# Kernel optimization log

Hardware: AMD Instinct MI355X
Metric: run time of the kernel (lower is better)

Reference implementation:

```python
import jax, jax.numpy as jnp
import numpy as np

HID = 256   # hiddenDims
QD = 64     # queryDims
B = 16      # number of segments
LQ = 2048   # query tokens per segment
LH = 2048   # key/value tokens per segment
EPS = 1e-5


def _layer_norm(x, w, b):
    m = jnp.mean(x, axis=-1, keepdims=True)
    v = jnp.mean((x - m) ** 2, axis=-1, keepdims=True)
    return (x - m) / jnp.sqrt(v + EPS) * w + b


def setup_inputs() -> dict:
    key = jax.random.key(0)
    ks = jax.random.split(key, 8)
    q = jax.random.normal(ks[0], (B * LQ, HID), jnp.float32)
    h = jax.random.normal(ks[1], (B * LH, HID), jnp.float32)
    s = 1.0 / np.sqrt(HID)
    WQ = jax.random.normal(ks[2], (QD, HID), jnp.float32) * s
    WK = jax.random.normal(ks[3], (QD, HID), jnp.float32) * s
    WV = jax.random.normal(ks[4], (HID, HID), jnp.float32) * s
    fc_w = jax.random.normal(ks[5], (HID, HID), jnp.float32) * s
    fc_b = jax.random.normal(ks[6], (HID,), jnp.float32) * 0.01
    norm0_w = jnp.ones((HID,), jnp.float32)
    norm0_b = jnp.zeros((HID,), jnp.float32)
    norm1_w = jnp.ones((HID,), jnp.float32)
    norm1_b = jnp.zeros((HID,), jnp.float32)
    qlens = jnp.full((B,), LQ, jnp.int32)
    hlens = jnp.full((B,), LH, jnp.int32)
    return {"q": q, "h": h, "WQ": WQ, "WK": WK, "WV": WV,
            "fc_w": fc_w, "fc_b": fc_b,
            "norm0_w": norm0_w, "norm0_b": norm0_b,
            "norm1_w": norm1_w, "norm1_b": norm1_b,
            "qlens": qlens, "hlens": hlens}


def reference(q, h, WQ, WK, WV, fc_w, fc_b,
              norm0_w, norm0_b, norm1_w, norm1_b, qlens, hlens):
    # segments are equal-length, so the ragged per-segment loop is exactly
    # batched block-diagonal attention over [B, L, D] views.
    nb = qlens.shape[0]
    Lq = q.shape[0] // nb
    Lh = h.shape[0] // hlens.shape[0]
    D = q.shape[-1]
    qq = (q @ WQ.T).reshape(nb, Lq, -1)          # [B, Lq, QD]
    k = (h @ WK.T).reshape(nb, Lh, -1)           # [B, Lh, QD]
    v = (h @ WV.T).reshape(nb, Lh, D)            # [B, Lh, D]
    scale = 1.0 / jnp.sqrt(jnp.asarray(qq.shape[-1], jnp.float32))
    a = jax.nn.softmax(jnp.einsum('bqc,bkc->bqk', qq, k) * scale, axis=-1)
    att = jnp.einsum('bqk,bkd->bqd', a, v).reshape(-1, D)  # concat of segments
    x = _layer_norm(q + att, norm0_w, norm0_b)
    hres = x @ fc_w.T + fc_b
    return _layer_norm(x + jax.nn.relu(hres), norm1_w, norm1_b)
```

## Files before the change

### kernel.cpp

```cpp
#include <hip/hip_runtime.h>
#include <hip/hip_bf16.h>

#define HID 256
#define QD 64
#define NSEG 16
#define SLQ 2048
#define SLH 2048


typedef __attribute__((ext_vector_type(8))) short bf16x8;
typedef __attribute__((ext_vector_type(8))) __bf16 bf16x8b;
typedef __attribute__((ext_vector_type(4))) float f32x4;
typedef __attribute__((ext_vector_type(4))) short s16x4;

#define BAR_LDS() asm volatile("s_waitcnt lgkmcnt(0)\n\ts_barrier" ::: "memory")

static __device__ __forceinline__ f32x4 mfma16(bf16x8 a, bf16x8 b, f32x4 c) {
  return __builtin_amdgcn_mfma_f32_16x16x32_bf16(
      __builtin_bit_cast(bf16x8b, a), __builtin_bit_cast(bf16x8b, b), c, 0, 0, 0);
}

static __device__ __forceinline__ short f2bf(float x) {
  union { float f; unsigned u; } v; v.f = x;
  unsigned r = v.u + 0x7fffu + ((v.u >> 16) & 1u);
  return (short)(r >> 16);
}

static __device__ __forceinline__ float bf2f(short s) {
  union { unsigned u; float f; } v;
  v.u = ((unsigned)(unsigned short)s) << 16;
  return v.f;
}

static __device__ __forceinline__ void pack_w(const float* __restrict__ s,
                                              short* __restrict__ d, int i) {
  int j = i & 7, l16 = (i >> 3) & 15, quad = (i >> 7) & 3, ks = (i >> 9) & 7,
      n = i >> 12;
  d[i] = f2bf(s[(size_t)(n * 16 + l16) * HID + ks * 32 + quad * 8 + j]);
}

__global__ __launch_bounds__(256) void cast4_kernel(const float* __restrict__ s0, short* __restrict__ d0, int n0,
                                                    const float* __restrict__ s1, short* __restrict__ d1, int n1,
                                                    const float* __restrict__ s2, short* __restrict__ d2, int n2,
                                                    const float* __restrict__ s3, short* __restrict__ d3, int n3) {
  int i = blockIdx.x * 256 + threadIdx.x;
  if (i < n0) pack_w(s0, d0, i);
  int j = i - n0;
  if (j >= 0 && j < n1) pack_w(s1, d1, j);
  int k = j - n1;
  if (k >= 0 && k < n2) pack_w(s2, d2, k);
  int l = k - n2;
  if (l >= 0 && l < n3) pack_w(s3, d3, l);
}

__global__ __launch_bounds__(256, 4) void proj_kernel(const float* __restrict__ q,
                                                      const float* __restrict__ h,
                                                      const short* __restrict__ wqb,
                                                      const short* __restrict__ wkb,
                                                      const short* __restrict__ wvb,
                                                      short* __restrict__ qq,
                                                      short* __restrict__ kb,
                                                      short* __restrict__ vt) {
  __shared__ short hb[64][264];
  int wave = threadIdx.x >> 6, lane = threadIdx.x & 63;
  int quad = lane >> 4, l16 = lane & 15;
  int mw = wave * 16;

  if (blockIdx.x < 512) {
    int m0 = blockIdx.x * 64;
#pragma unroll
    for (int i = 0; i < 16; ++i) {
      int idx = i * 256 + threadIdx.x;
      int row = idx >> 6, col = (idx & 63) * 4;
      f32x4 v = *(const f32x4*)(h + (size_t)(m0 + row) * HID + col);
      s16x4 pk;
#pragma unroll
      for (int j = 0; j < 4; ++j) pk[j] = f2bf(v[j]);
      *(s16x4*)&hb[row][col] = pk;
    }
    __syncthreads();
    f32x4 kacc[4];
    f32x4 vacc[16];
#pragma unroll
    for (int n = 0; n < 4; ++n) kacc[n] = f32x4{0.f, 0.f, 0.f, 0.f};
#pragma unroll
    for (int n = 0; n < 16; ++n) vacc[n] = f32x4{0.f, 0.f, 0.f, 0.f};
#pragma unroll
    for (int ks = 0; ks < 8; ++ks) {
      bf16x8 a = *(const bf16x8*)&hb[mw + l16][ks * 32 + quad * 8];
#pragma unroll
      for (int n = 0; n < 4; ++n) {
        bf16x8 b = *(const bf16x8*)(wkb + (size_t)((n * 8 + ks) * 64 + lane) * 8);
        kacc[n] = mfma16(a, b, kacc[n]);
      }
#pragma unroll
      for (int mt = 0; mt < 16; ++mt) {
        bf16x8 wf = *(const bf16x8*)(wvb + (size_t)((mt * 8 + ks) * 64 + lane) * 8);
        vacc[mt] = mfma16(wf, a, vacc[mt]);
      }
    }
    {
      char* kx = (char*)&hb[mw][0];
#pragma unroll
      for (int n = 0; n < 4; ++n)
#pragma unroll
        for (int r = 0; r < 4; ++r) {
          int k16 = quad * 4 + r;
          int bo = (k16 * 128 + (n * 16 + l16) * 2) ^ ((k16 & 7) << 4);
          *(short*)(kx + bo) = f2bf(kacc[n][r]);
        }
      asm volatile("s_waitcnt lgkmcnt(0)" ::: "memory");
      int seg = (m0 + mw) >> 11;
      int g = ((m0 + mw) & 2047) >> 4;
      short* kdst = kb + (size_t)seg * 131072 + (size_t)g * 1024 + lane * 8;
#pragma unroll
      for (int p = 0; p < 2; ++p) {
        int bo = (l16 * 128 + p * 64 + quad * 16) ^ ((l16 & 7) << 4);
        *(bf16x8*)(kdst + p * 512) = *(bf16x8*)(kx + bo);
      }
    }
    __syncthreads();
    {
      char* vbuf = (char*)&hb[0][0];
#pragma unroll
      for (int mt = 0; mt < 16; ++mt)
#pragma unroll
        for (int r = 0; r < 4; ++r) {
          int dv = mt * 16 + quad * 4 + r;
          int bo = (dv * 128 + (mw + l16) * 2) ^ ((dv & 7) << 4);
          *(short*)(vbuf + bo) = f2bf(vacc[mt][r]);
        }
      __syncthreads();
      int seg = m0 >> 11;
      int t0 = m0 & 2047;
      int kt = t0 >> 7;
      int ksb = (t0 >> 5) & 3;
      short* vdst = vt + (size_t)seg * 524288;
#pragma unroll
      for (int i = 0; i < 8; ++i) {
        int u = wave * 8 + i;
        int ksl = u >> 4, d16 = u & 15;
        int dim = d16 * 16 + l16;
        int bo = (dim * 128 + ksl * 64 + quad * 16) ^ ((dim & 7) << 4);
        size_t unit = (size_t)((kt * 4 + ksb + ksl) * 16 + d16);
        *(bf16x8*)(vdst + unit * 512 + lane * 8) = *(bf16x8*)(vbuf + bo);
      }
    }
  } else {
    int m0 = (blockIdx.x - 512) * 64;
#pragma unroll
    for (int i = 0; i < 16; ++i) {
      int idx = i * 256 + threadIdx.x;
      int row = idx >> 6, col = (idx & 63) * 4;
      f32x4 v = *(const f32x4*)(q + (size_t)(m0 + row) * HID + col);
      s16x4 pk;
#pragma unroll
      for (int j = 0; j < 4; ++j) pk[j] = f2bf(v[j]);
      *(s16x4*)&hb[row][col] = pk;
    }
    __syncthreads();
    f32x4 acc[4];
#pragma unroll
    for (int n = 0; n < 4; ++n) acc[n] = f32x4{0.f, 0.f, 0.f, 0.f};
#pragma unroll
    for (int ks = 0; ks < 8; ++ks) {
      bf16x8 a = *(const bf16x8*)&hb[mw + l16][ks * 32 + quad * 8];
#pragma unroll
      for (int n = 0; n < 4; ++n) {
        bf16x8 b = *(const bf16x8*)(wqb + (size_t)((n * 8 + ks) * 64 + lane) * 8);
        acc[n] = mfma16(a, b, acc[n]);
      }
    }
    {
      char* kx = (char*)&hb[mw][0];
#pragma unroll
      for (int n = 0; n < 4; ++n)
#pragma unroll
        for (int r = 0; r < 4; ++r) {
          int k16 = quad * 4 + r;
          int bo = (k16 * 128 + (n * 16 + l16) * 2) ^ ((k16 & 7) << 4);
          *(short*)(kx + bo) = f2bf(acc[n][r]);
        }
      asm volatile("s_waitcnt lgkmcnt(0)" ::: "memory");
      int g = (m0 >> 4) + wave;
      short* qdst = qq + (size_t)g * 1024 + lane * 8;
#pragma unroll
      for (int p = 0; p < 2; ++p) {
        int bo = (l16 * 128 + p * 64 + quad * 16) ^ ((l16 & 7) << 4);
        *(bf16x8*)(qdst + p * 512) = *(bf16x8*)(kx + bo);
      }
    }
  }
}

__global__ __launch_bounds__(512, 4) void attn_kernel(const short* __restrict__ qq,
                                                      const short* __restrict__ kb,
                                                      const short* __restrict__ vt,
                                                      const float* __restrict__ qres,
                                                      const float* __restrict__ n0w,
                                                      const float* __restrict__ n0b,
                                                      short* __restrict__ xb) {
  __shared__ short p_lds[2][64][136];
  __shared__ float plsum[4][2][16];
  int wave = threadIdx.x >> 6, lane = threadIdx.x & 63;
  int quad = lane >> 4, l16 = lane & 15;
  int qg = wave >> 1, kh = wave & 1;
  int b = blockIdx.x;
  int xcd = b & 7, li = b >> 3;
  int seg = xcd * 2 + (li >> 5);
  int tile = li & 31;
  int qrow0 = seg * SLQ + tile * 64;
  const short* kseg = kb + (size_t)seg * 131072;
  const short* vseg = vt + (size_t)seg * 524288;

  const short* qbase = qq + (size_t)((qrow0 >> 4) + qg) * 1024 + lane * 8;
  bf16x8 qf0 = *(const bf16x8*)qbase;
  bf16x8 qf1 = *(const bf16x8*)(qbase + 512);

  f32x4 o[4][2];
#pragma unroll
  for (int m = 0; m < 4; ++m)
#pragma unroll
    for (int n = 0; n < 2; ++n) o[m][n] = f32x4{0.f, 0.f, 0.f, 0.f};
  float lsum = 0.f;
  const float cexp = 0.125f * 1.44269504f;
  bf16x8 kpre[4][2];

#define LOADK(KT)                                                               \
  {                                                                             \
    _Pragma("unroll") for (int t = 0; t < 4; ++t) {                             \
      const short* kp = kseg + (size_t)((KT) * 8 + kh * 4 + t) * 1024 + lane * 8;\
      kpre[t][0] = *(const bf16x8*)kp;                                          \
      kpre[t][1] = *(const bf16x8*)(kp + 512);                                  \
    }                                                                           \
  }

#define S_PHASE(BUF)                                                            \
  {                                                                             \
    f32x4 s[4];                                                                 \
    _Pragma("unroll") for (int t = 0; t < 4; ++t) {                             \
      f32x4 a = f32x4{0.f, 0.f, 0.f, 0.f};                                      \
      a = mfma16(kpre[t][0], qf0, a);                                           \
      a = mfma16(kpre[t][1], qf1, a);                                           \
      s[t] = a;                                                                 \
    }                                                                           \
    _Pragma("unroll") for (int t = 0; t < 4; ++t) {                             \
      float p0 = __builtin_amdgcn_exp2f(s[t][0] * cexp);                        \
      float p1 = __builtin_amdgcn_exp2f(s[t][1] * cexp);                        \
      float p2 = __builtin_amdgcn_exp2f(s[t][2] * cexp);                        \
      float p3 = __builtin_amdgcn_exp2f(s[t][3] * cexp);                        \
      lsum += (p0 + p1) + (p2 + p3);                                            \
      s16x4 pk;                                                                 \
      pk[0] = f2bf(p0); pk[1] = f2bf(p1); pk[2] = f2bf(p2); pk[3] = f2bf(p3);   \
      *(s16x4*)&p_lds[BUF][qg * 16 + l16][kh * 64 + t * 16 + quad * 4] = pk;    \
    }                                                                           \
  }

#define PV_PHASE(KT, BUF)                                                       \
  {                                                                             \
    _Pragma("unroll") for (int ks = 0; ks < 4; ++ks) {                          \
      bf16x8 pf[4];                                                             \
      _Pragma("unroll") for (int m = 0; m < 4; ++m)                             \
        pf[m] = *(const bf16x8*)&p_lds[BUF][m * 16 + l16][ks * 32 + quad * 8];  \
      _Pragma("unroll") for (int n = 0; n < 2; ++n) {                           \
        const short* vp = vseg +                                                \
            ((size_t)((KT) * 4 + ks) * 16 + wave * 2 + n) * 512 + lane * 8;     \
        bf16x8 vf = *(const bf16x8*)vp;                                         \
        _Pragma("unroll") for (int m = 0; m < 4; ++m)                           \
          o[m][n] = mfma16(pf[m], vf, o[m][n]);                                 \
      }                                                                         \
    }                                                                           \
  }

  LOADK(tile & 15)
  S_PHASE(0)
  LOADK((tile + 1) & 15)
  BAR_LDS();
#pragma unroll 1
  for (int j = 1; j < 16; ++j) {
    S_PHASE(j & 1)
    if (j < 15) LOADK((tile + j + 1) & 15)
    PV_PHASE((tile + j - 1) & 15, (j - 1) & 1)
    BAR_LDS();
  }
  PV_PHASE((tile + 15) & 15, 1)

  lsum += __shfl_xor(lsum, 16);
  lsum += __shfl_xor(lsum, 32);

  BAR_LDS();
  if (lane < 16) plsum[qg][kh][lane] = lsum;
  short (*ob)[264] = (short(*)[264]) & p_lds[0][0][0];
#pragma unroll
  for (int m = 0; m < 4; ++m)
#pragma unroll
    for (int n = 0; n < 2; ++n)
#pragma unroll
      for (int r = 0; r < 4; ++r)
        ob[m * 16 + quad * 4 + r][wave * 32 + n * 16 + l16] = f2bf(o[m][n][r]);
  BAR_LDS();

  {
    int row = wave * 8 + (lane >> 3);
    int c0 = (lane & 7) * 32;
    float linv = 1.f / (plsum[row >> 4][0][row & 15] + plsum[row >> 4][1][row & 15]);
    float y[32];
    float s1 = 0.f, s2 = 0.f;
    const float* qp = qres + (size_t)(qrow0 + row) * HID + c0;
#pragma unroll
    for (int k = 0; k < 4; ++k) {
      bf16x8 ov = *(const bf16x8*)&ob[row][c0 + k * 8];
      f32x4 qa = *(const f32x4*)(qp + k * 8);
      f32x4 qb = *(const f32x4*)(qp + k * 8 + 4);
#pragma unroll
      for (int j = 0; j < 4; ++j) {
        float yv = qa[j] + bf2f(ov[j]) * linv;
        y[k * 8 + j] = yv;
        s1 += yv; s2 += yv * yv;
      }
#pragma unroll
      for (int j = 0; j < 4; ++j) {
        float yv = qb[j] + bf2f(ov[4 + j]) * linv;
        y[k * 8 + 4 + j] = yv;
        s1 += yv; s2 += yv * yv;
      }
    }
    s1 += __shfl_xor(s1, 1); s2 += __shfl_xor(s2, 1);
    s1 += __shfl_xor(s1, 2); s2 += __shfl_xor(s2, 2);
    s1 += __shfl_xor(s1, 4); s2 += __shfl_xor(s2, 4);
    float mean = s1 * (1.f / HID);
    float var = s2 * (1.f / HID) - mean * mean;
    float rstd = rsqrtf(var + 1e-5f);
    short* xp = xb + (size_t)(qrow0 + row) * HID + c0;
#pragma unroll
    for (int k = 0; k < 4; ++k) {
      f32x4 wa = *(const f32x4*)(n0w + c0 + k * 8);
      f32x4 wb = *(const f32x4*)(n0w + c0 + k * 8 + 4);
      f32x4 ba = *(const f32x4*)(n0b + c0 + k * 8);
      f32x4 bb = *(const f32x4*)(n0b + c0 + k * 8 + 4);
      s16x4 o0, o1;
#pragma unroll
      for (int j = 0; j < 4; ++j) {
        o0[j] = f2bf((y[k * 8 + j] - mean) * rstd * wa[j] + ba[j]);
        o1[j] = f2bf((y[k * 8 + 4 + j] - mean) * rstd * wb[j] + bb[j]);
      }
      *(s16x4*)(xp + k * 8) = o0;
      *(s16x4*)(xp + k * 8 + 4) = o1;
    }
  }
#undef LOADK
#undef S_PHASE
#undef PV_PHASE
}

__global__ __launch_bounds__(256) void fc_ln_kernel(const short* __restrict__ xb,
                                                    const short* __restrict__ fwb,
                                                    const float* __restrict__ fcb,
                                                    const float* __restrict__ w1,
                                                    const float* __restrict__ b1,
                                                    float* __restrict__ out) {
  __shared__ short xt[64][264];
  int m0 = blockIdx.x * 64;
#pragma unroll
  for (int i = 0; i < 8; ++i) {
    int idx = i * 256 + threadIdx.x;
    int row = idx >> 5, col = (idx & 31) * 8;
    bf16x8 v = *(const bf16x8*)(xb + (size_t)(m0 + row) * HID + col);
    *(bf16x8*)&xt[row][col] = v;
  }
  __syncthreads();
  int wave = threadIdx.x >> 6, lane = threadIdx.x & 63;
  int quad = lane >> 4, l16 = lane & 15;
  int mw = wave * 16;
  f32x4 acc[16];
#pragma unroll
  for (int n = 0; n < 16; ++n) acc[n] = f32x4{0.f, 0.f, 0.f, 0.f};
#pragma unroll
  for (int ks = 0; ks < 8; ++ks) {
    bf16x8 a = *(const bf16x8*)&xt[mw + l16][ks * 32 + quad * 8];
#pragma unroll
    for (int n = 0; n < 16; ++n) {
      bf16x8 b = *(const bf16x8*)(fwb + (size_t)((n * 8 + ks) * 64 + lane) * 8);
      acc[n] = mfma16(a, b, acc[n]);
    }
  }
#pragma unroll
  for (int r = 0; r < 4; ++r) {
    int lrow = mw + quad * 4 + r;
    int row = m0 + lrow;
    float yv[16];
    float s = 0.f, s2 = 0.f;
#pragma unroll
    for (int n = 0; n < 16; ++n) {
      int col = n * 16 + l16;
      float hres = acc[n][r] + fcb[col];
      hres = fmaxf(hres, 0.f);
      float y = bf2f(xt[lrow][col]) + hres;
      yv[n] = y;
      s += y;
      s2 += y * y;
    }
#pragma unroll
    for (int off = 1; off < 16; off <<= 1) {
      s += __shfl_xor(s, off);
      s2 += __shfl_xor(s2, off);
    }
    float mean = s * (1.f / HID);
    float var = s2 * (1.f / HID) - mean * mean;
    float rstd = rsqrtf(var + 1e-5f);
#pragma unroll
    for (int n = 0; n < 16; ++n) {
      int col = n * 16 + l16;
      out[(size_t)row * HID + col] = (yv[n] - mean) * rstd * w1[col] + b1[col];
    }
  }
}

extern "C" void kernel_launch(void* const* d_in, const int* in_sizes, int n_in,
                              void* d_out, int out_size, void* d_ws, size_t ws_size,
                              hipStream_t stream) {
  const float* q = (const float*)d_in[0];
  const float* h = (const float*)d_in[1];
  const float* WQ = (const float*)d_in[2];
  const float* WK = (const float*)d_in[3];
  const float* WV = (const float*)d_in[4];
  const float* fc_w = (const float*)d_in[5];
  const float* fc_b = (const float*)d_in[6];
  const float* n0w = (const float*)d_in[7];
  const float* n0b = (const float*)d_in[8];
  const float* n1w = (const float*)d_in[9];
  const float* n1b = (const float*)d_in[10];

  char* ws = (char*)d_ws;
  short* qq = (short*)(ws);
  short* kb = (short*)(ws + ((size_t)4 << 20));
  short* vt = (short*)(ws + ((size_t)8 << 20));
  short* xb = (short*)(ws + ((size_t)24 << 20));
  short* wqb = (short*)(ws + ((size_t)40 << 20));
  short* wkb = (short*)(ws + ((size_t)40 << 20) + 32 * 1024);
  short* wvb = (short*)(ws + ((size_t)40 << 20) + 64 * 1024);
  short* fwb = (short*)(ws + ((size_t)40 << 20) + 192 * 1024);

  cast4_kernel<<<640, 256, 0, stream>>>(WQ, wqb, QD * HID, WK, wkb, QD * HID,
                                        WV, wvb, HID * HID, fc_w, fwb, HID * HID);
  proj_kernel<<<1024, 256, 0, stream>>>(q, h, wqb, wkb, wvb, qq, kb, vt);
  attn_kernel<<<512, 512, 0, stream>>>(qq, kb, vt, q, n0w, n0b, xb);
  fc_ln_kernel<<<512, 256, 0, stream>>>(xb, fwb, fc_b, n1w, n1b, (float*)d_out);
}
```

Measured before the change: 271.9 us.

## Fuse Q projection and FC+LayerNorm epilogue into attention kernel

Moves the query projection out of the projection kernel into the attention kernel's prologue, where each block projects its own 64 query rows through LDS. The fc GEMM, ReLU, residual and second LayerNorm are folded into the attention epilogue, with row statistics reduced across wave halves through shared memory, and the separate fc_ln kernel is removed. This drops one launch plus the round trips of the qq and xb intermediates through global memory. In exchange the attention kernel uses more LDS and registers, which may lower occupancy and lengthen its serial prologue and epilogue.

```diff
diff --git a/kernel.cpp b/kernel.cpp
--- a/kernel.cpp
+++ b/kernel.cpp
@@ -53,155 +53,111 @@
   if (l >= 0 && l < n3) pack_w(s3, d3, l);
 }
 
-__global__ __launch_bounds__(256, 4) void proj_kernel(const float* __restrict__ q,
-                                                      const float* __restrict__ h,
-                                                      const short* __restrict__ wqb,
-                                                      const short* __restrict__ wkb,
-                                                      const short* __restrict__ wvb,
-                                                      short* __restrict__ qq,
-                                                      short* __restrict__ kb,
-                                                      short* __restrict__ vt) {
+__global__ __launch_bounds__(256, 4) void proj_kv_kernel(const float* __restrict__ h,
+                                                         const short* __restrict__ wkb,
+                                                         const short* __restrict__ wvb,
+                                                         short* __restrict__ kb,
+                                                         short* __restrict__ vt) {
   __shared__ short hb[64][264];
   int wave = threadIdx.x >> 6, lane = threadIdx.x & 63;
   int quad = lane >> 4, l16 = lane & 15;
   int mw = wave * 16;
-
-  if (blockIdx.x < 512) {
-    int m0 = blockIdx.x * 64;
-#pragma unroll
-    for (int i = 0; i < 16; ++i) {
-      int idx = i * 256 + threadIdx.x;
-      int row = idx >> 6, col = (idx & 63) * 4;
-      f32x4 v = *(const f32x4*)(h + (size_t)(m0 + row) * HID + col);
-      s16x4 pk;
-#pragma unroll
-      for (int j = 0; j < 4; ++j) pk[j] = f2bf(v[j]);
-      *(s16x4*)&hb[row][col] = pk;
-    }
+  int m0 = blockIdx.x * 64;
+#pragma unroll
+  for (int i = 0; i < 16; ++i) {
+    int idx = i * 256 + threadIdx.x;
+    int row = idx >> 6, col = (idx & 63) * 4;
+    f32x4 v = *(const f32x4*)(h + (size_t)(m0 + row) * HID + col);
+    s16x4 pk;
+#pragma unroll
+    for (int j = 0; j < 4; ++j) pk[j] = f2bf(v[j]);
+    *(s16x4*)&hb[row][col] = pk;
+  }
+  __syncthreads();
+  f32x4 kacc[4];
+  f32x4 vacc[16];
+#pragma unroll
+  for (int n = 0; n < 4; ++n) kacc[n] = f32x4{0.f, 0.f, 0.f, 0.f};
+#pragma unroll
+  for (int n = 0; n < 16; ++n) vacc[n] = f32x4{0.f, 0.f, 0.f, 0.f};
+#pragma unroll
+  for (int ks = 0; ks < 8; ++ks) {
+    bf16x8 a = *(const bf16x8*)&hb[mw + l16][ks * 32 + quad * 8];
+#pragma unroll
+    for (int n = 0; n < 4; ++n) {
+      bf16x8 b = *(const bf16x8*)(wkb + (size_t)((n * 8 + ks) * 64 + lane) * 8);
+      kacc[n] = mfma16(a, b, kacc[n]);
+    }
+#pragma unroll
+    for (int mt = 0; mt < 16; ++mt) {
+      bf16x8 wf = *(const bf16x8*)(wvb + (size_t)((mt * 8 + ks) * 64 + lane) * 8);
+      vacc[mt] = mfma16(wf, a, vacc[mt]);
+    }
+  }
+  {
+    char* kx = (char*)&hb[mw][0];
+#pragma unroll
+    for (int n = 0; n < 4; ++n)
+#pragma unroll
+      for (int r = 0; r < 4; ++r) {
+        int k16 = quad * 4 + r;
+        int bo = (k16 * 128 + (n * 16 + l16) * 2) ^ ((k16 & 7) << 4);
+        *(short*)(kx + bo) = f2bf(kacc[n][r]);
+      }
+    asm volatile("s_waitcnt lgkmcnt(0)" ::: "memory");
+    int seg = (m0 + mw) >> 11;
+    int g = ((m0 + mw) & 2047) >> 4;
+    short* kdst = kb + (size_t)seg * 131072 + (size_t)g * 1024 + lane * 8;
+#pragma unroll
+    for (int p = 0; p < 2; ++p) {
+      int bo = (l16 * 128 + p * 64 + quad * 16) ^ ((l16 & 7) << 4);
+      *(bf16x8*)(kdst + p * 512) = *(bf16x8*)(kx + bo);
+    }
+  }
+  __syncthreads();
+  {
+    char* vbuf = (char*)&hb[0][0];
+#pragma unroll
+    for (int mt = 0; mt < 16; ++mt)
+#pragma unroll
+      for (int r = 0; r < 4; ++r) {
+        int dv = mt * 16 + quad * 4 + r;
+        int bo = (dv * 128 + (mw + l16) * 2) ^ ((dv & 7) << 4);
+        *(short*)(vbuf + bo) = f2bf(vacc[mt][r]);
+      }
     __syncthreads();
-    f32x4 kacc[4];
-    f32x4 vacc[16];
-#pragma unroll
-    for (int n = 0; n < 4; ++n) kacc[n] = f32x4{0.f, 0.f, 0.f, 0.f};
-#pragma unroll
-    for (int n = 0; n < 16; ++n) vacc[n] = f32x4{0.f, 0.f, 0.f, 0.f};
-#pragma unroll
-    for (int ks = 0; ks < 8; ++ks) {
-      bf16x8 a = *(const bf16x8*)&hb[mw + l16][ks * 32 + quad * 8];
-#pragma unroll
-      for (int n = 0; n < 4; ++n) {
-        bf16x8 b = *(const bf16x8*)(wkb + (size_t)((n * 8 + ks) * 64 + lane) * 8);
-        kacc[n] = mfma16(a, b, kacc[n]);
-      }
-#pragma unroll
-      for (int mt = 0; mt < 16; ++mt) {
-        bf16x8 wf = *(const bf16x8*)(wvb + (size_t)((mt * 8 + ks) * 64 + lane) * 8);
-        vacc[mt] = mfma16(wf, a, vacc[mt]);
-      }
-    }
-    {
-      char* kx = (char*)&hb[mw][0];
-#pragma unroll
-      for (int n = 0; n < 4; ++n)
-#pragma unroll
-        for (int r = 0; r < 4; ++r) {
-          int k16 = quad * 4 + r;
-          int bo = (k16 * 128 + (n * 16 + l16) * 2) ^ ((k16 & 7) << 4);
-          *(short*)(kx + bo) = f2bf(kacc[n][r]);
-        }
-      asm volatile("s_waitcnt lgkmcnt(0)" ::: "memory");
-      int seg = (m0 + mw) >> 11;
-      int g = ((m0 + mw) & 2047) >> 4;
-      short* kdst = kb + (size_t)seg * 131072 + (size_t)g * 1024 + lane * 8;
-#pragma unroll
-      for (int p = 0; p < 2; ++p) {
-        int bo = (l16 * 128 + p * 64 + quad * 16) ^ ((l16 & 7) << 4);
-        *(bf16x8*)(kdst + p * 512) = *(bf16x8*)(kx + bo);
-      }
-    }
-    __syncthreads();
-    {
-      char* vbuf = (char*)&hb[0][0];
-#pragma unroll
-      for (int mt = 0; mt < 16; ++mt)
-#pragma unroll
-        for (int r = 0; r < 4; ++r) {
-          int dv = mt * 16 + quad * 4 + r;
-          int bo = (dv * 128 + (mw + l16) * 2) ^ ((dv & 7) << 4);
-          *(short*)(vbuf + bo) = f2bf(vacc[mt][r]);
-        }
-      __syncthreads();
-      int seg = m0 >> 11;
-      int t0 = m0 & 2047;
-      int kt = t0 >> 7;
-      int ksb = (t0 >> 5) & 3;
-      short* vdst = vt + (size_t)seg * 524288;
-#pragma unroll
-      for (int i = 0; i < 8; ++i) {
-        int u = wave * 8 + i;
-        int ksl = u >> 4, d16 = u & 15;
-        int dim = d16 * 16 + l16;
-        int bo = (dim * 128 + ksl * 64 + quad * 16) ^ ((dim & 7) << 4);
-        size_t unit = (size_t)((kt * 4 + ksb + ksl) * 16 + d16);
-        *(bf16x8*)(vdst + unit * 512 + lane * 8) = *(bf16x8*)(vbuf + bo);
-      }
-    }
-  } else {
-    int m0 = (blockIdx.x - 512) * 64;
-#pragma unroll
-    for (int i = 0; i < 16; ++i) {
-      int idx = i * 256 + threadIdx.x;
-      int row = idx >> 6, col = (idx & 63) * 4;
-      f32x4 v = *(const f32x4*)(q + (size_t)(m0 + row) * HID + col);
-      s16x4 pk;
-#pragma unroll
-      for (int j = 0; j < 4; ++j) pk[j] = f2bf(v[j]);
-      *(s16x4*)&hb[row][col] = pk;
-    }
-    __syncthreads();
-    f32x4 acc[4];
-#pragma unroll
-    for (int n = 0; n < 4; ++n) acc[n] = f32x4{0.f, 0.f, 0.f, 0.f};
-#pragma unroll
-    for (int ks = 0; ks < 8; ++ks) {
-      bf16x8 a = *(const bf16x8*)&hb[mw + l16][ks * 32 + quad * 8];
-#pragma unroll
-      for (int n = 0; n < 4; ++n) {
-        bf16x8 b = *(const bf16x8*)(wqb + (size_t)((n * 8 + ks) * 64 + lane) * 8);
-        acc[n] = mfma16(a, b, acc[n]);
-      }
-    }
-    {
-      char* kx = (char*)&hb[mw][0];
-#pragma unroll
-      for (int n = 0; n < 4; ++n)
-#pragma unroll
-        for (int r = 0; r < 4; ++r) {
-          int k16 = quad * 4 + r;
-          int bo = (k16 * 128 + (n * 16 + l16) * 2) ^ ((k16 & 7) << 4);
-          *(short*)(kx + bo) = f2bf(acc[n][r]);
-        }
-      asm volatile("s_waitcnt lgkmcnt(0)" ::: "memory");
-      int g = (m0 >> 4) + wave;
-      short* qdst = qq + (size_t)g * 1024 + lane * 8;
-#pragma unroll
-      for (int p = 0; p < 2; ++p) {
-        int bo = (l16 * 128 + p * 64 + quad * 16) ^ ((l16 & 7) << 4);
-        *(bf16x8*)(qdst + p * 512) = *(bf16x8*)(kx + bo);
-      }
-    }
-  }
-}
-
-__global__ __launch_bounds__(512, 4) void attn_kernel(const short* __restrict__ qq,
+    int seg = m0 >> 11;
+    int t0 = m0 & 2047;
+    int kt = t0 >> 7;
+    int ksb = (t0 >> 5) & 3;
+    short* vdst = vt + (size_t)seg * 524288;
+#pragma unroll
+    for (int i = 0; i < 8; ++i) {
+      int u = wave * 8 + i;
+      int ksl = u >> 4, d16 = u & 15;
+      int dim = d16 * 16 + l16;
+      int bo = (dim * 128 + ksl * 64 + quad * 16) ^ ((dim & 7) << 4);
+      size_t unit = (size_t)((kt * 4 + ksb + ksl) * 16 + d16);
+      *(bf16x8*)(vdst + unit * 512 + lane * 8) = *(bf16x8*)(vbuf + bo);
+    }
+  }
+}
+
+__global__ __launch_bounds__(512, 4) void attn_kernel(const float* __restrict__ q,
+                                                      const short* __restrict__ wqb,
                                                       const short* __restrict__ kb,
                                                       const short* __restrict__ vt,
-                                                      const float* __restrict__ qres,
+                                                      const short* __restrict__ fwb,
+                                                      const float* __restrict__ fcb,
                                                       const float* __restrict__ n0w,
                                                       const float* __restrict__ n0b,
-                                                      short* __restrict__ xb) {
+                                                      const float* __restrict__ n1w,
+                                                      const float* __restrict__ n1b,
+                                                      float* __restrict__ out) {
   __shared__ short p_lds[2][64][136];
+  __shared__ short qx[4096];
   __shared__ float plsum[4][2][16];
+  __shared__ float rs[2][2][64];
   int wave = threadIdx.x >> 6, lane = threadIdx.x & 63;
   int quad = lane >> 4, l16 = lane & 15;
   int qg = wave >> 1, kh = wave & 1;
@@ -213,16 +169,6 @@
   const short* kseg = kb + (size_t)seg * 131072;
   const short* vseg = vt + (size_t)seg * 524288;
 
-  const short* qbase = qq + (size_t)((qrow0 >> 4) + qg) * 1024 + lane * 8;
-  bf16x8 qf0 = *(const bf16x8*)qbase;
-  bf16x8 qf1 = *(const bf16x8*)(qbase + 512);
-
-  f32x4 o[4][2];
-#pragma unroll
-  for (int m = 0; m < 4; ++m)
-#pragma unroll
-    for (int n = 0; n < 2; ++n) o[m][n] = f32x4{0.f, 0.f, 0.f, 0.f};
-  float lsum = 0.f;
   const float cexp = 0.125f * 1.44269504f;
   bf16x8 kpre[4][2];
 
@@ -234,6 +180,59 @@
       kpre[t][1] = *(const bf16x8*)(kp + 512);                                  \
     }                                                                           \
   }
+
+  LOADK(tile & 15)
+
+  short (*st)[264] = (short(*)[264]) & p_lds[0][0][0];
+  bf16x8 qf0, qf1;
+  {
+    const float* qsrc = q + (size_t)qrow0 * HID;
+#pragma unroll
+    for (int i = 0; i < 8; ++i) {
+      int idx = i * 512 + threadIdx.x;
+      int row = idx >> 6, col = (idx & 63) * 4;
+      f32x4 v = *(const f32x4*)(qsrc + (size_t)row * HID + col);
+      s16x4 pk;
+#pragma unroll
+      for (int j = 0; j < 4; ++j) pk[j] = f2bf(v[j]);
+      *(s16x4*)&st[row][col] = pk;
+    }
+    __syncthreads();
+    f32x4 qacc[2];
+    qacc[0] = f32x4{0.f, 0.f, 0.f, 0.f};
+    qacc[1] = f32x4{0.f, 0.f, 0.f, 0.f};
+#pragma unroll
+    for (int ks = 0; ks < 8; ++ks) {
+      bf16x8 a = *(const bf16x8*)&st[qg * 16 + l16][ks * 32 + quad * 8];
+#pragma unroll
+      for (int ni = 0; ni < 2; ++ni) {
+        int n = kh * 2 + ni;
+        bf16x8 wb = *(const bf16x8*)(wqb + (size_t)((n * 8 + ks) * 64 + lane) * 8);
+        qacc[ni] = mfma16(a, wb, qacc[ni]);
+      }
+    }
+    BAR_LDS();
+#pragma unroll
+    for (int ni = 0; ni < 2; ++ni)
+#pragma unroll
+      for (int r = 0; r < 4; ++r) {
+        int n = kh * 2 + ni;
+        int colp = (n & 1) * 16 + l16;
+        qx[(qg * 2 + (n >> 1)) * 512 + ((colp >> 3) * 16 + quad * 4 + r) * 8 +
+           (colp & 7)] = f2bf(qacc[ni][r]);
+      }
+    BAR_LDS();
+    const short* qxp = qx + qg * 1024 + lane * 8;
+    qf0 = *(const bf16x8*)qxp;
+    qf1 = *(const bf16x8*)(qxp + 512);
+  }
+
+  f32x4 o[4][2];
+#pragma unroll
+  for (int m = 0; m < 4; ++m)
+#pragma unroll
+    for (int n = 0; n < 2; ++n) o[m][n] = f32x4{0.f, 0.f, 0.f, 0.f};
+  float lsum = 0.f;
 
 #define S_PHASE(BUF)                                                            \
   {                                                                             \
@@ -272,7 +271,6 @@
     }                                                                           \
   }
 
-  LOADK(tile & 15)
   S_PHASE(0)
   LOADK((tile + 1) & 15)
   BAR_LDS();
@@ -306,7 +304,7 @@
     float linv = 1.f / (plsum[row >> 4][0][row & 15] + plsum[row >> 4][1][row & 15]);
     float y[32];
     float s1 = 0.f, s2 = 0.f;
-    const float* qp = qres + (size_t)(qrow0 + row) * HID + c0;
+    const float* qp = q + (size_t)(qrow0 + row) * HID + c0;
 #pragma unroll
     for (int k = 0; k < 4; ++k) {
       bf16x8 ov = *(const bf16x8*)&ob[row][c0 + k * 8];
@@ -331,7 +329,6 @@
     float mean = s1 * (1.f / HID);
     float var = s2 * (1.f / HID) - mean * mean;
     float rstd = rsqrtf(var + 1e-5f);
-    short* xp = xb + (size_t)(qrow0 + row) * HID + c0;
 #pragma unroll
     for (int k = 0; k < 4; ++k) {
       f32x4 wa = *(const f32x4*)(n0w + c0 + k * 8);
@@ -344,76 +341,65 @@
         o0[j] = f2bf((y[k * 8 + j] - mean) * rstd * wa[j] + ba[j]);
         o1[j] = f2bf((y[k * 8 + 4 + j] - mean) * rstd * wb[j] + bb[j]);
       }
-      *(s16x4*)(xp + k * 8) = o0;
-      *(s16x4*)(xp + k * 8 + 4) = o1;
+      *(s16x4*)&ob[row][c0 + k * 8] = o0;
+      *(s16x4*)&ob[row][c0 + k * 8 + 4] = o1;
+    }
+  }
+  BAR_LDS();
+
+  {
+    f32x4 facc[8];
+#pragma unroll
+    for (int n2 = 0; n2 < 8; ++n2) facc[n2] = f32x4{0.f, 0.f, 0.f, 0.f};
+#pragma unroll
+    for (int ks = 0; ks < 8; ++ks) {
+      bf16x8 a = *(const bf16x8*)&ob[qg * 16 + l16][ks * 32 + quad * 8];
+#pragma unroll
+      for (int n2 = 0; n2 < 8; ++n2) {
+        int n = kh * 8 + n2;
+        bf16x8 wb = *(const bf16x8*)(fwb + (size_t)((n * 8 + ks) * 64 + lane) * 8);
+        facc[n2] = mfma16(a, wb, facc[n2]);
+      }
+    }
+#pragma unroll
+    for (int r = 0; r < 4; ++r) {
+      int row = qg * 16 + quad * 4 + r;
+      float s = 0.f, s2 = 0.f;
+#pragma unroll
+      for (int n2 = 0; n2 < 8; ++n2) {
+        int col = kh * 128 + n2 * 16 + l16;
+        float hres = fmaxf(facc[n2][r] + fcb[col], 0.f);
+        float yv = bf2f(ob[row][col]) + hres;
+        s += yv; s2 += yv * yv;
+      }
+      s += __shfl_xor(s, 1); s2 += __shfl_xor(s2, 1);
+      s += __shfl_xor(s, 2); s2 += __shfl_xor(s2, 2);
+      s += __shfl_xor(s, 4); s2 += __shfl_xor(s2, 4);
+      s += __shfl_xor(s, 8); s2 += __shfl_xor(s2, 8);
+      if (l16 == 0) { rs[0][kh][row] = s; rs[1][kh][row] = s2; }
+    }
+    BAR_LDS();
+#pragma unroll
+    for (int r = 0; r < 4; ++r) {
+      int row = qg * 16 + quad * 4 + r;
+      float st1 = rs[0][0][row] + rs[0][1][row];
+      float st2 = rs[1][0][row] + rs[1][1][row];
+      float mean = st1 * (1.f / HID);
+      float var = st2 * (1.f / HID) - mean * mean;
+      float rstd = rsqrtf(var + 1e-5f);
+      float* op = out + (size_t)(qrow0 + row) * HID;
+#pragma unroll
+      for (int n2 = 0; n2 < 8; ++n2) {
+        int col = kh * 128 + n2 * 16 + l16;
+        float hres = fmaxf(facc[n2][r] + fcb[col], 0.f);
+        float yv = bf2f(ob[row][col]) + hres;
+        op[col] = (yv - mean) * rstd * n1w[col] + n1b[col];
+      }
     }
   }
 #undef LOADK
 #undef S_PHASE
 #undef PV_PHASE
-}
-
-__global__ __launch_bounds__(256) void fc_ln_kernel(const short* __restrict__ xb,
-                                                    const short* __restrict__ fwb,
-                                                    const float* __restrict__ fcb,
-                                                    const float* __restrict__ w1,
-                                                    const float* __restrict__ b1,
-                                                    float* __restrict__ out) {
-  __shared__ short xt[64][264];
-  int m0 = blockIdx.x * 64;
-#pragma unroll
-  for (int i = 0; i < 8; ++i) {
-    int idx = i * 256 + threadIdx.x;
-    int row = idx >> 5, col = (idx & 31) * 8;
-    bf16x8 v = *(const bf16x8*)(xb + (size_t)(m0 + row) * HID + col);
-    *(bf16x8*)&xt[row][col] = v;
-  }
-  __syncthreads();
-  int wave = threadIdx.x >> 6, lane = threadIdx.x & 63;
-  int quad = lane >> 4, l16 = lane & 15;
-  int mw = wave * 16;
-  f32x4 acc[16];
-#pragma unroll
-  for (int n = 0; n < 16; ++n) acc[n] = f32x4{0.f, 0.f, 0.f, 0.f};
-#pragma unroll
-  for (int ks = 0; ks < 8; ++ks) {
-    bf16x8 a = *(const bf16x8*)&xt[mw + l16][ks * 32 + quad * 8];
-#pragma unroll
-    for (int n = 0; n < 16; ++n) {
-      bf16x8 b = *(const bf16x8*)(fwb + (size_t)((n * 8 + ks) * 64 + lane) * 8);
-      acc[n] = mfma16(a, b, acc[n]);
-    }
-  }
-#pragma unroll
-  for (int r = 0; r < 4; ++r) {
-    int lrow = mw + quad * 4 + r;
-    int row = m0 + lrow;
-    float yv[16];
-    float s = 0.f, s2 = 0.f;
-#pragma unroll
-    for (int n = 0; n < 16; ++n) {
-      int col = n * 16 + l16;
-      float hres = acc[n][r] + fcb[col];
-      hres = fmaxf(hres, 0.f);
-      float y = bf2f(xt[lrow][col]) + hres;
-      yv[n] = y;
-      s += y;
-      s2 += y * y;
-    }
-#pragma unroll
-    for (int off = 1; off < 16; off <<= 1) {
-      s += __shfl_xor(s, off);
-      s2 += __shfl_xor(s2, off);
-    }
-    float mean = s * (1.f / HID);
-    float var = s2 * (1.f / HID) - mean * mean;
-    float rstd = rsqrtf(var + 1e-5f);
-#pragma unroll
-    for (int n = 0; n < 16; ++n) {
-      int col = n * 16 + l16;
-      out[(size_t)row * HID + col] = (yv[n] - mean) * rstd * w1[col] + b1[col];
-    }
-  }
 }
 
 extern "C" void kernel_launch(void* const* d_in, const int* in_sizes, int n_in,
@@ -432,18 +418,16 @@
   const float* n1b = (const float*)d_in[10];
 
   char* ws = (char*)d_ws;
-  short* qq = (short*)(ws);
-  short* kb = (short*)(ws + ((size_t)4 << 20));
-  short* vt = (short*)(ws + ((size_t)8 << 20));
-  short* xb = (short*)(ws + ((size_t)24 << 20));
-  short* wqb = (short*)(ws + ((size_t)40 << 20));
-  short* wkb = (short*)(ws + ((size_t)40 << 20) + 32 * 1024);
-  short* wvb = (short*)(ws + ((size_t)40 << 20) + 64 * 1024);
-  short* fwb = (short*)(ws + ((size_t)40 << 20) + 192 * 1024);
+  short* kb = (short*)(ws);
+  short* vt = (short*)(ws + ((size_t)4 << 20));
+  short* wqb = (short*)(ws + ((size_t)20 << 20));
+  short* wkb = (short*)(ws + ((size_t)20 << 20) + 32 * 1024);
+  short* wvb = (short*)(ws + ((size_t)20 << 20) + 64 * 1024);
+  short* fwb = (short*)(ws + ((size_t)20 << 20) + 192 * 1024);
 
   cast4_kernel<<<640, 256, 0, stream>>>(WQ, wqb, QD * HID, WK, wkb, QD * HID,
                                         WV, wvb, HID * HID, fc_w, fwb, HID * HID);
-  proj_kernel<<<1024, 256, 0, stream>>>(q, h, wqb, wkb, wvb, qq, kb, vt);
-  attn_kernel<<<512, 512, 0, stream>>>(qq, kb, vt, q, n0w, n0b, xb);
-  fc_ln_kernel<<<512, 256, 0, stream>>>(xb, fwb, fc_b, n1w, n1b, (float*)d_out);
-}
+  proj_kv_kernel<<<512, 256, 0, stream>>>(h, wkb, wvb, kb, vt);
+  attn_kernel<<<512, 512, 0, stream>>>(q, wqb, kb, vt, fwb, fc_b,
+                                       n0w, n0b, n1w, n1b, (float*)d_out);
+}
```

Result: faster. 245.2 us (-9.8%).
